# Optimization experiments

Hardware: AMD Instinct MI355X
Metric: run time of the kernel (lower is better)

Reference implementation:

```python
import jax, jax.numpy as jnp
import numpy as np

N_NODES = 20000
NC = 16
NUM_BASIS = 5
MAX_CENTER = 3.5

# Real-basis Clebsch-Gordan tensors C[m, m_f, m_o] for the (l, l_f) -> l_o paths.
# Real l=1 basis ordered (m=-1,0,1) = (y,z,x); (y,z,x) is a cyclic permutation of
# (x,y,z) so the standard Levi-Civita gives the 1x1->1 coupling.
_C000 = np.ones((1, 1, 1), dtype=np.float32)
_C011 = np.eye(3, dtype=np.float32).reshape(1, 3, 3)
_C101 = np.eye(3, dtype=np.float32).reshape(3, 1, 3)
_C110 = (np.eye(3, dtype=np.float32) / np.sqrt(3.0)).reshape(3, 3, 1)
_eps = np.zeros((3, 3, 3), dtype=np.float32)
for (i, j, k) in [(0, 1, 2), (1, 2, 0), (2, 0, 1)]:
    _eps[i, j, k] = 1.0
    _eps[i, k, j] = -1.0
_C111 = (_eps / np.sqrt(2.0)).astype(np.float32)

Y00 = 0.28209479177387814  # 1 / (2 sqrt(pi))
Y1C = 0.4886025119029199   # sqrt(3 / (4 pi))


def _spherical_filter(edges, coeffs, l_f):
    """SphericalFilter.__call__: RBF radial part x solid harmonics. -> [E, n_c, 2l_f+1]."""
    centers = jnp.linspace(0.0, MAX_CENTER, NUM_BASIS)
    spread = (MAX_CENTER - 0.0) / NUM_BASIS  # (max - min) / num_basis = 0.7
    radius = jnp.linalg.norm(edges, ord=2, axis=-1)              # [E]
    rbfs = jnp.exp(-spread * (radius[:, None] - centers) ** 2)   # [E, num_basis]
    rad = rbfs @ coeffs.T                                        # [E, n_c]
    if l_f == 0:
        y = jnp.full(edges.shape[:-1] + (1,), Y00, dtype=edges.dtype)
    else:  # l_f == 1: solid harmonics r^1 * Y_1m, order (y, z, x)
        y = Y1C * edges[:, jnp.array([1, 2, 0])]
    y = jnp.nan_to_num(y)
    return rad[:, :, None] * y[:, None, :]


def _tp(nodes, filt, cg, w):
    """Depthwise CG tensor product: [E,c,m],[E,c,f],[m,f,o] -> w[c] * [E,c,o]."""
    out = jnp.einsum('ecm,ecf,mfo->eco', nodes, filt, jnp.asarray(cg))
    return w[None, :, None] * out


def setup_inputs() -> dict:
    key = jax.random.key(0)
    ks = jax.random.split(key, 16)
    E = 640000
    inp = {
        'coords': jax.random.normal(ks[0], (N_NODES, 3), dtype=jnp.float32),
        'nodes0': jax.random.normal(ks[1], (N_NODES, NC, 1), dtype=jnp.float32),
        'nodes1': jax.random.normal(ks[2], (N_NODES, NC, 3), dtype=jnp.float32),
        'edges': jax.random.normal(ks[3], (E, 3), dtype=jnp.float32),
        'senders': jax.random.randint(ks[4], (E,), 0, N_NODES, dtype=jnp.int32),
        'receivers': jax.random.randint(ks[5], (E,), 0, N_NODES, dtype=jnp.int32),
        'coeffs_00': jax.random.uniform(ks[6], (NC, NUM_BASIS), dtype=jnp.float32),
        'coeffs_01': jax.random.uniform(ks[7], (NC, NUM_BASIS), dtype=jnp.float32),
        'coeffs_10': jax.random.uniform(ks[8], (NC, NUM_BASIS), dtype=jnp.float32),
        'coeffs_11': jax.random.uniform(ks[9], (NC, NUM_BASIS), dtype=jnp.float32),
        'w_000': jax.random.normal(ks[10], (NC,), dtype=jnp.float32) + 1.0,
        'w_011': jax.random.normal(ks[11], (NC,), dtype=jnp.float32) + 1.0,
        'w_101': jax.random.normal(ks[12], (NC,), dtype=jnp.float32) + 1.0,
        'w_110': jax.random.normal(ks[13], (NC,), dtype=jnp.float32) + 1.0,
        'w_111': jax.random.normal(ks[14], (NC,), dtype=jnp.float32) + 1.0,
    }
    return inp


def reference(coords, nodes0, nodes1, edges, senders, receivers,
              coeffs_00, coeffs_01, coeffs_10, coeffs_11,
              w_000, w_011, w_101, w_110, w_111):
    # Gather sender node features once per l.
    n0s = nodes0[senders]  # [E, NC, 1]
    n1s = nodes1[senders]  # [E, NC, 3]

    # Filters (loop order: l=0 filters [l_f=0, l_f=1], then l=1 filters).
    f00 = _spherical_filter(edges, coeffs_00, 0)  # [E, NC, 1]
    f01 = _spherical_filter(edges, coeffs_01, 1)  # [E, NC, 3]
    f10 = _spherical_filter(edges, coeffs_10, 0)  # [E, NC, 1]
    f11 = _spherical_filter(edges, coeffs_11, 1)  # [E, NC, 3]

    # Tensor-product messages, concatenated per output degree along channels.
    # l_o = 0 paths: (l=0, l_f=0), (l=1, l_f=1)
    m0 = jnp.concatenate([
        _tp(n0s, f00, _C000, w_000),
        _tp(n1s, f11, _C110, w_110),
    ], axis=-2)  # [E, 2*NC, 1]
    # l_o = 1 paths: (0,1), (1,0), (1,1)
    m1 = jnp.concatenate([
        _tp(n0s, f01, _C011, w_011),
        _tp(n1s, f10, _C101, w_101),
        _tp(n1s, f11, _C111, w_111),
    ], axis=-2)  # [E, 3*NC, 3]

    new0 = jax.ops.segment_sum(m0, receivers, num_segments=N_NODES)
    new1 = jax.ops.segment_sum(m1, receivers, num_segments=N_NODES)
    return coords, new0, new1
```

## Files before the change

### kernel.cpp

```cpp
#include <hip/hip_runtime.h>
#include <hip/hip_fp16.h>

#define E_EDGES 640000
#define NN 20000
#define NC 16
#define PBIN 64

#define Y00F 0.28209479177387814f
#define Y1CF 0.4886025119029199f
#define RS3  0.5773502691896258f
#define RS2  0.7071067811865476f

typedef float nf4 __attribute__((ext_vector_type(4)));

struct Acc {
    float a000, a110;
    float a011x, a011y, a011z;
    float a101x, a101y, a101z;
    float a111x, a111y, a111z;
};

__device__ __forceinline__ unsigned pack2h(float a, float b) {
    unsigned short ua = __half_as_ushort(__float2half(a));
    unsigned short ub = __half_as_ushort(__float2half(b));
    return (unsigned)ua | ((unsigned)ub << 16);
}
__device__ __forceinline__ float lo_h(unsigned u) {
    return __half2float(__ushort_as_half((unsigned short)(u & 0xffffu)));
}
__device__ __forceinline__ float hi_h(unsigned u) {
    return __half2float(__ushort_as_half((unsigned short)(u >> 16)));
}


__global__ void init1_kernel(const float* __restrict__ coords,
                             float* __restrict__ out,
                             int* __restrict__ cnt,
                             int* __restrict__ ovf_count) {
    int i = blockIdx.x * blockDim.x + threadIdx.x;
    if (i < 3 * NN) out[i] = coords[i];
    if (i < NN) cnt[i] = 0;
    if (i == 0) *ovf_count = 0;
}

__global__ void bin_kernel(const float* __restrict__ edges,
                           const int* __restrict__ senders,
                           const int* __restrict__ receivers,
                           int* __restrict__ cnt,
                           nf4* __restrict__ bins,
                           int* __restrict__ ovf_count,
                           int* __restrict__ ovf_list) {
    int e = blockIdx.x * blockDim.x + threadIdx.x;
    if (e >= E_EDGES) return;
    float ex = edges[3 * e + 0];
    float ey = edges[3 * e + 1];
    float ez = edges[3 * e + 2];
    int s  = senders[e];
    int rc = receivers[e];
    int pos = atomicAdd(&cnt[rc], 1);
    if (pos < PBIN) {
        float r2 = ex * ex + ey * ey + ez * ez;
        float r  = sqrtf(r2);
        float A  = __expf(-0.7f * r2);
        float t  = __expf(1.225f * r);
        nf4 rec;
        rec.x = __uint_as_float(pack2h(Y1CF * ey, Y1CF * ez));
        rec.y = __uint_as_float(pack2h(Y1CF * ex, t));
        rec.z = A;
        rec.w = __int_as_float(s);
        bins[(size_t)rc * PBIN + pos] = rec;
    } else {
        int k = atomicAdd(ovf_count, 1);
        if (k < 4096) ovf_list[k] = e;
    }
}

__global__ __launch_bounds__(256) void gather1_kernel(
    const nf4*    __restrict__ bins,
    const int*    __restrict__ cnt,
    const float*  __restrict__ nodes0,
    const float*  __restrict__ nodes1,
    const float*  __restrict__ c00, const float* __restrict__ c01,
    const float*  __restrict__ c10, const float* __restrict__ c11,
    const float*  __restrict__ w000, const float* __restrict__ w011,
    const float*  __restrict__ w101, const float* __restrict__ w110,
    const float*  __restrict__ w111,
    float* __restrict__ out0, float* __restrict__ out1)
{
    int gtid = blockIdx.x * blockDim.x + threadIdx.x;
    int node = gtid >> 6;
    int lane = threadIdx.x & 63;
    int c    = lane & 15;
    int j    = lane >> 4;
    if (node >= NN) return;

    const float KB[5] = {1.0f, 0.58512723f, 0.11721218f, 0.00803909f, 1.8876652e-4f};
    float k00[5], k01[5], k10[5], k11[5];
#pragma unroll
    for (int b = 0; b < 5; b++) {
        k00[b] = c00[c * 5 + b] * KB[b];
        k01[b] = c01[c * 5 + b] * KB[b];
        k10[b] = c10[c * 5 + b] * KB[b];
        k11[b] = c11[c * 5 + b] * KB[b];
    }

    int n = cnt[node];
    n = (n < PBIN) ? n : PBIN;
    const nf4* base = bins + (size_t)node * PBIN;

    Acc A = {};

#define HORNER(k, t) fmaf((t), fmaf((t), fmaf((t), fmaf((t), k[4], k[3]), k[2]), k[1]), k[0])
#define BODY(rec)                                                          \
    {                                                                      \
        unsigned u0 = __float_as_uint(rec.x);                              \
        unsigned u1 = __float_as_uint(rec.y);                              \
        float py = lo_h(u0), pz = hi_h(u0);                                \
        float px = lo_h(u1), tf = hi_h(u1);                                \
        float Af = rec.z;                                                  \
        int s = __float_as_int(rec.w);                                     \
        float rad00 = Af * HORNER(k00, tf);                                \
        float rad01 = Af * HORNER(k01, tf);                                \
        float rad10 = Af * HORNER(k10, tf);                                \
        float rad11 = Af * HORNER(k11, tf);                                \
        float n0 = nodes0[s * NC + c];                                     \
        const float* n1p = nodes1 + (s * NC + c) * 3;                      \
        float n1a = n1p[0], n1b = n1p[1], n1c = n1p[2];                    \
        A.a000 = fmaf(n0, rad00, A.a000);                                  \
        A.a110 = fmaf(rad11, n1a * py + n1b * pz + n1c * px, A.a110);      \
        float kA = n0 * rad01;                                             \
        A.a011x = fmaf(kA, py, A.a011x);                                   \
        A.a011y = fmaf(kA, pz, A.a011y);                                   \
        A.a011z = fmaf(kA, px, A.a011z);                                   \
        A.a101x = fmaf(rad10, n1a, A.a101x);                               \
        A.a101y = fmaf(rad10, n1b, A.a101y);                               \
        A.a101z = fmaf(rad10, n1c, A.a101z);                               \
        A.a111x = fmaf(rad11, n1b * px - n1c * pz, A.a111x);               \
        A.a111y = fmaf(rad11, n1c * py - n1a * px, A.a111y);               \
        A.a111z = fmaf(rad11, n1a * pz - n1b * py, A.a111z);               \
    }

    int i = j;
    for (; i + 12 < n; i += 16) {
        nf4 r0 = __builtin_nontemporal_load(&base[i]);
        nf4 r1 = __builtin_nontemporal_load(&base[i + 4]);
        nf4 r2 = __builtin_nontemporal_load(&base[i + 8]);
        nf4 r3 = __builtin_nontemporal_load(&base[i + 12]);
        BODY(r0);
        BODY(r1);
        BODY(r2);
        BODY(r3);
    }
    for (; i < n; i += 4) {
        nf4 r0 = __builtin_nontemporal_load(&base[i]);
        BODY(r0);
    }
#undef BODY
#undef HORNER

#define RED(v) v += __shfl_xor(v, 16, 64); v += __shfl_xor(v, 32, 64)
    RED(A.a000); RED(A.a110);
    RED(A.a011x); RED(A.a011y); RED(A.a011z);
    RED(A.a101x); RED(A.a101y); RED(A.a101z);
    RED(A.a111x); RED(A.a111y); RED(A.a111z);
#undef RED

    if (j == 0) {
        float s000 = w000[c] * Y00F;
        float s110 = w110[c] * RS3;
        float s011 = w011[c];
        float s101 = w101[c] * Y00F;
        float s111 = w111[c] * RS2;

        out0[node * 32 + c]      = s000 * A.a000;
        out0[node * 32 + 16 + c] = s110 * A.a110;

        float* o1 = out1 + node * 144;
        o1[3 * c + 0] = s011 * A.a011x;
        o1[3 * c + 1] = s011 * A.a011y;
        o1[3 * c + 2] = s011 * A.a011z;
        o1[3 * (16 + c) + 0] = s101 * A.a101x;
        o1[3 * (16 + c) + 1] = s101 * A.a101y;
        o1[3 * (16 + c) + 2] = s101 * A.a101z;
        o1[3 * (32 + c) + 0] = s111 * A.a111x;
        o1[3 * (32 + c) + 1] = s111 * A.a111y;
        o1[3 * (32 + c) + 2] = s111 * A.a111z;
    }
}

__global__ void cleanup_kernel(
    const int* __restrict__ ovf_count, const int* __restrict__ ovf_list,
    const float* __restrict__ edges, const int* __restrict__ senders,
    const int* __restrict__ receivers,
    const float* __restrict__ nodes0, const float* __restrict__ nodes1,
    const float* __restrict__ c00, const float* __restrict__ c01,
    const float* __restrict__ c10, const float* __restrict__ c11,
    const float* __restrict__ w000, const float* __restrict__ w011,
    const float* __restrict__ w101, const float* __restrict__ w110,
    const float* __restrict__ w111,
    float* __restrict__ out0, float* __restrict__ out1)
{
    int nov = *ovf_count;
    if (nov > 4096) nov = 4096;
    for (int k = threadIdx.x; k < nov; k += blockDim.x) {
        int e = ovf_list[k];
        float ex = edges[3 * e + 0], ey = edges[3 * e + 1], ez = edges[3 * e + 2];
        float r = sqrtf(ex * ex + ey * ey + ez * ez);
        float rbf[5];
#pragma unroll
        for (int b = 0; b < 5; b++) {
            float d = r - 0.875f * (float)b;
            rbf[b] = __expf(-0.7f * d * d);
        }
        int s = senders[e], rc = receivers[e];
        const float* n0p = nodes0 + s * NC;
        const float* n1p = nodes1 + s * NC * 3;
        float* o0 = out0 + rc * 32;
        float* o1 = out1 + rc * 144;
        float pey = Y1CF * ey, pez = Y1CF * ez, pex = Y1CF * ex;
        for (int c = 0; c < NC; c++) {
            float rad00 = 0.f, rad01 = 0.f, rad10 = 0.f, rad11 = 0.f;
#pragma unroll
            for (int b = 0; b < 5; b++) {
                rad00 = fmaf(rbf[b], c00[c * 5 + b], rad00);
                rad01 = fmaf(rbf[b], c01[c * 5 + b], rad01);
                rad10 = fmaf(rbf[b], c10[c * 5 + b], rad10);
                rad11 = fmaf(rbf[b], c11[c * 5 + b], rad11);
            }
            float n0 = n0p[c];
            float n1a = n1p[3 * c + 0], n1b = n1p[3 * c + 1], n1c = n1p[3 * c + 2];
            float f11a = rad11 * pey, f11b = rad11 * pez, f11c = rad11 * pex;
            atomicAdd(&o0[c], w000[c] * n0 * rad00 * Y00F);
            atomicAdd(&o0[16 + c], w110[c] * RS3 * (n1a * f11a + n1b * f11b + n1c * f11c));
            float kA = w011[c] * n0 * rad01;
            atomicAdd(&o1[3 * c + 0], kA * pey);
            atomicAdd(&o1[3 * c + 1], kA * pez);
            atomicAdd(&o1[3 * c + 2], kA * pex);
            float kB = w101[c] * rad10 * Y00F;
            atomicAdd(&o1[3 * (16 + c) + 0], kB * n1a);
            atomicAdd(&o1[3 * (16 + c) + 1], kB * n1b);
            atomicAdd(&o1[3 * (16 + c) + 2], kB * n1c);
            float kC = w111[c] * RS2;
            atomicAdd(&o1[3 * (32 + c) + 0], kC * (n1b * f11c - n1c * f11b));
            atomicAdd(&o1[3 * (32 + c) + 1], kC * (n1c * f11a - n1a * f11c));
            atomicAdd(&o1[3 * (32 + c) + 2], kC * (n1a * f11b - n1b * f11a));
        }
    }
}

__global__ void init_out_fb(const float* __restrict__ coords,
                            float* __restrict__ out, int out_size) {
    int i = blockIdx.x * blockDim.x + threadIdx.x;
    if (i < 3 * NN) out[i] = coords[i];
    else if (i < out_size) out[i] = 0.0f;
}

__global__ __launch_bounds__(256) void tp_edges_fb(
    const float* __restrict__ edges, const int* __restrict__ senders,
    const int* __restrict__ receivers, const float* __restrict__ nodes0,
    const float* __restrict__ nodes1,
    const float* __restrict__ c00, const float* __restrict__ c01,
    const float* __restrict__ c10, const float* __restrict__ c11,
    const float* __restrict__ w000, const float* __restrict__ w011,
    const float* __restrict__ w101, const float* __restrict__ w110,
    const float* __restrict__ w111,
    float* __restrict__ out0, float* __restrict__ out1) {
    int e = blockIdx.x * blockDim.x + threadIdx.x;
    if (e >= E_EDGES) return;
    float ex = edges[3 * e + 0], ey = edges[3 * e + 1], ez = edges[3 * e + 2];
    float r = sqrtf(ex * ex + ey * ey + ez * ez);
    float rbf[5];
#pragma unroll
    for (int b = 0; b < 5; b++) {
        float d = r - 0.875f * (float)b;
        rbf[b] = __expf(-0.7f * d * d);
    }
    int s = senders[e], rc = receivers[e];
    const float* n0p = nodes0 + s * NC;
    const float* n1p = nodes1 + s * NC * 3;
    float* o0 = out0 + rc * 32;
    float* o1 = out1 + rc * 144;
    float pey = Y1CF * ey, pez = Y1CF * ez, pex = Y1CF * ex;
    for (int c = 0; c < NC; c++) {
        float rad00 = 0.f, rad01 = 0.f, rad10 = 0.f, rad11 = 0.f;
#pragma unroll
        for (int b = 0; b < 5; b++) {
            rad00 = fmaf(rbf[b], c00[c * 5 + b], rad00);
            rad01 = fmaf(rbf[b], c01[c * 5 + b], rad01);
            rad10 = fmaf(rbf[b], c10[c * 5 + b], rad10);
            rad11 = fmaf(rbf[b], c11[c * 5 + b], rad11);
        }
        float n0 = n0p[c];
        float n1a = n1p[3 * c + 0], n1b = n1p[3 * c + 1], n1c = n1p[3 * c + 2];
        float f11a = rad11 * pey, f11b = rad11 * pez, f11c = rad11 * pex;
        atomicAdd(&o0[c], w000[c] * n0 * rad00 * Y00F);
        atomicAdd(&o0[16 + c], w110[c] * RS3 * (n1a * f11a + n1b * f11b + n1c * f11c));
        float kA = w011[c] * n0 * rad01;
        atomicAdd(&o1[3 * c + 0], kA * pey);
        atomicAdd(&o1[3 * c + 1], kA * pez);
        atomicAdd(&o1[3 * c + 2], kA * pex);
        float kB = w101[c] * rad10 * Y00F;
        atomicAdd(&o1[3 * (16 + c) + 0], kB * n1a);
        atomicAdd(&o1[3 * (16 + c) + 1], kB * n1b);
        atomicAdd(&o1[3 * (16 + c) + 2], kB * n1c);
        float kC = w111[c] * RS2;
        atomicAdd(&o1[3 * (32 + c) + 0], kC * (n1b * f11c - n1c * f11b));
        atomicAdd(&o1[3 * (32 + c) + 1], kC * (n1c * f11a - n1a * f11c));
        atomicAdd(&o1[3 * (32 + c) + 2], kC * (n1a * f11b - n1b * f11a));
    }
}

extern "C" void kernel_launch(void* const* d_in, const int* in_sizes, int n_in,
                              void* d_out, int out_size, void* d_ws, size_t ws_size,
                              hipStream_t stream) {
    const float* coords    = (const float*)d_in[0];
    const float* nodes0    = (const float*)d_in[1];
    const float* nodes1    = (const float*)d_in[2];
    const float* edges     = (const float*)d_in[3];
    const int*   senders   = (const int*)  d_in[4];
    const int*   receivers = (const int*)  d_in[5];
    const float* c00       = (const float*)d_in[6];
    const float* c01       = (const float*)d_in[7];
    const float* c10       = (const float*)d_in[8];
    const float* c11       = (const float*)d_in[9];
    const float* w000      = (const float*)d_in[10];
    const float* w011      = (const float*)d_in[11];
    const float* w101      = (const float*)d_in[12];
    const float* w110      = (const float*)d_in[13];
    const float* w111      = (const float*)d_in[14];

    float* out  = (float*)d_out;
    float* out0 = out + 3 * NN;
    float* out1 = out + 3 * NN + NN * 2 * NC;

    size_t bins_bytes = (size_t)NN * PBIN * 16;
    size_t need1 = bins_bytes + (size_t)(NN + 1 + 4096) * 4;

    if (ws_size >= need1) {
        nf4* bins      = (nf4*)d_ws;
        int* cnt       = (int*)((char*)d_ws + bins_bytes);
        int* ovf_count = cnt + NN;
        int* ovf_list  = ovf_count + 1;

        init1_kernel<<<(3 * NN + 255) / 256, 256, 0, stream>>>(coords, out, cnt, ovf_count);
        bin_kernel<<<(E_EDGES + 255) / 256, 256, 0, stream>>>(
            edges, senders, receivers, cnt, bins, ovf_count, ovf_list);
        gather1_kernel<<<(NN * 64 + 255) / 256, 256, 0, stream>>>(
            bins, cnt, nodes0, nodes1,
            c00, c01, c10, c11, w000, w011, w101, w110, w111, out0, out1);
        cleanup_kernel<<<1, 256, 0, stream>>>(
            ovf_count, ovf_list, edges, senders, receivers, nodes0, nodes1,
            c00, c01, c10, c11, w000, w011, w101, w110, w111, out0, out1);
    } else {
        init_out_fb<<<(out_size + 255) / 256, 256, 0, stream>>>(coords, out, out_size);
        tp_edges_fb<<<(E_EDGES + 255) / 256, 256, 0, stream>>>(
            edges, senders, receivers, nodes0, nodes1,
            c00, c01, c10, c11, w000, w011, w101, w110, w111, out0, out1);
    }
}
```

Before: 173.5 us.

## Pack node features to fp16 and use 128 threads per node in gather

Result: faster. 165.4 us (-4.7%).

```diff
diff --git a/kernel.cpp b/kernel.cpp
--- a/kernel.cpp
+++ b/kernel.cpp
@@ -12,13 +12,7 @@
 #define RS2  0.7071067811865476f
 
 typedef float nf4 __attribute__((ext_vector_type(4)));
-
-struct Acc {
-    float a000, a110;
-    float a011x, a011y, a011z;
-    float a101x, a101y, a101z;
-    float a111x, a111y, a111z;
-};
+typedef unsigned int nu2 __attribute__((ext_vector_type(2)));
 
 __device__ __forceinline__ unsigned pack2h(float a, float b) {
     unsigned short ua = __half_as_ushort(__float2half(a));
@@ -34,13 +28,24 @@
 
 
 __global__ void init1_kernel(const float* __restrict__ coords,
+                             const float* __restrict__ nodes0,
+                             const float* __restrict__ nodes1,
                              float* __restrict__ out,
                              int* __restrict__ cnt,
-                             int* __restrict__ ovf_count) {
+                             int* __restrict__ ovf_count,
+                             nu2* __restrict__ nodes_h) {
     int i = blockIdx.x * blockDim.x + threadIdx.x;
     if (i < 3 * NN) out[i] = coords[i];
     if (i < NN) cnt[i] = 0;
     if (i == 0) *ovf_count = 0;
+    if (i < NN * NC) {
+        float n0 = nodes0[i];
+        const float* n1p = nodes1 + i * 3;
+        nu2 v;
+        v.x = pack2h(n0, n1p[0]);
+        v.y = pack2h(n1p[1], n1p[2]);
+        nodes_h[i] = v;
+    }
 }
 
 __global__ void bin_kernel(const float* __restrict__ edges,
@@ -78,8 +83,7 @@
 __global__ __launch_bounds__(256) void gather1_kernel(
     const nf4*    __restrict__ bins,
     const int*    __restrict__ cnt,
-    const float*  __restrict__ nodes0,
-    const float*  __restrict__ nodes1,
+    const nu2*    __restrict__ nodes_h,
     const float*  __restrict__ c00, const float* __restrict__ c01,
     const float*  __restrict__ c10, const float* __restrict__ c11,
     const float*  __restrict__ w000, const float* __restrict__ w011,
@@ -87,12 +91,12 @@
     const float*  __restrict__ w111,
     float* __restrict__ out0, float* __restrict__ out1)
 {
-    int gtid = blockIdx.x * blockDim.x + threadIdx.x;
-    int node = gtid >> 6;
-    int lane = threadIdx.x & 63;
-    int c    = lane & 15;
-    int j    = lane >> 4;
-    if (node >= NN) return;
+    int t    = threadIdx.x;
+    int slot = t >> 7;
+    int node = blockIdx.x * 2 + slot;
+    int tid  = t & 127;
+    int c    = tid & 15;
+    int j    = tid >> 4;
 
     const float KB[5] = {1.0f, 0.58512723f, 0.11721218f, 0.00803909f, 1.8876652e-4f};
     float k00[5], k01[5], k10[5], k11[5];
@@ -108,7 +112,10 @@
     n = (n < PBIN) ? n : PBIN;
     const nf4* base = bins + (size_t)node * PBIN;
 
-    Acc A = {};
+    float a000 = 0.f, a110 = 0.f;
+    float a011x = 0.f, a011y = 0.f, a011z = 0.f;
+    float a101x = 0.f, a101y = 0.f, a101z = 0.f;
+    float a111x = 0.f, a111y = 0.f, a111z = 0.f;
 
 #define HORNER(k, t) fmaf((t), fmaf((t), fmaf((t), fmaf((t), k[4], k[3]), k[2]), k[1]), k[0])
 #define BODY(rec)                                                          \
@@ -119,39 +126,35 @@
         float px = lo_h(u1), tf = hi_h(u1);                                \
         float Af = rec.z;                                                  \
         int s = __float_as_int(rec.w);                                     \
+        nu2 nh = nodes_h[s * NC + c];                                      \
         float rad00 = Af * HORNER(k00, tf);                                \
         float rad01 = Af * HORNER(k01, tf);                                \
         float rad10 = Af * HORNER(k10, tf);                                \
         float rad11 = Af * HORNER(k11, tf);                                \
-        float n0 = nodes0[s * NC + c];                                     \
-        const float* n1p = nodes1 + (s * NC + c) * 3;                      \
-        float n1a = n1p[0], n1b = n1p[1], n1c = n1p[2];                    \
-        A.a000 = fmaf(n0, rad00, A.a000);                                  \
-        A.a110 = fmaf(rad11, n1a * py + n1b * pz + n1c * px, A.a110);      \
+        float n0  = lo_h(nh.x), n1a = hi_h(nh.x);                          \
+        float n1b = lo_h(nh.y), n1c = hi_h(nh.y);                          \
+        a000 = fmaf(n0, rad00, a000);                                      \
+        a110 = fmaf(rad11, n1a * py + n1b * pz + n1c * px, a110);          \
         float kA = n0 * rad01;                                             \
-        A.a011x = fmaf(kA, py, A.a011x);                                   \
-        A.a011y = fmaf(kA, pz, A.a011y);                                   \
-        A.a011z = fmaf(kA, px, A.a011z);                                   \
-        A.a101x = fmaf(rad10, n1a, A.a101x);                               \
-        A.a101y = fmaf(rad10, n1b, A.a101y);                               \
-        A.a101z = fmaf(rad10, n1c, A.a101z);                               \
-        A.a111x = fmaf(rad11, n1b * px - n1c * pz, A.a111x);               \
-        A.a111y = fmaf(rad11, n1c * py - n1a * px, A.a111y);               \
-        A.a111z = fmaf(rad11, n1a * pz - n1b * py, A.a111z);               \
+        a011x = fmaf(kA, py, a011x);                                       \
+        a011y = fmaf(kA, pz, a011y);                                       \
+        a011z = fmaf(kA, px, a011z);                                       \
+        a101x = fmaf(rad10, n1a, a101x);                                   \
+        a101y = fmaf(rad10, n1b, a101y);                                   \
+        a101z = fmaf(rad10, n1c, a101z);                                   \
+        a111x = fmaf(rad11, n1b * px - n1c * pz, a111x);                   \
+        a111y = fmaf(rad11, n1c * py - n1a * px, a111y);                   \
+        a111z = fmaf(rad11, n1a * pz - n1b * py, a111z);                   \
     }
 
     int i = j;
-    for (; i + 12 < n; i += 16) {
+    for (; i + 8 < n; i += 16) {
         nf4 r0 = __builtin_nontemporal_load(&base[i]);
-        nf4 r1 = __builtin_nontemporal_load(&base[i + 4]);
-        nf4 r2 = __builtin_nontemporal_load(&base[i + 8]);
-        nf4 r3 = __builtin_nontemporal_load(&base[i + 12]);
+        nf4 r1 = __builtin_nontemporal_load(&base[i + 8]);
         BODY(r0);
         BODY(r1);
-        BODY(r2);
-        BODY(r3);
-    }
-    for (; i < n; i += 4) {
+    }
+    if (i < n) {
         nf4 r0 = __builtin_nontemporal_load(&base[i]);
         BODY(r0);
     }
@@ -159,32 +162,48 @@
 #undef HORNER
 
 #define RED(v) v += __shfl_xor(v, 16, 64); v += __shfl_xor(v, 32, 64)
-    RED(A.a000); RED(A.a110);
-    RED(A.a011x); RED(A.a011y); RED(A.a011z);
-    RED(A.a101x); RED(A.a101y); RED(A.a101z);
-    RED(A.a111x); RED(A.a111y); RED(A.a111z);
+    RED(a000); RED(a110);
+    RED(a011x); RED(a011y); RED(a011z);
+    RED(a101x); RED(a101y); RED(a101z);
+    RED(a111x); RED(a111y); RED(a111z);
 #undef RED
 
-    if (j == 0) {
+    __shared__ float red[2][16][11];
+    int half = tid >> 6;
+    if (half == 0 && (tid & 63) < 16) {
+        float* p = red[slot][c];
+        p[0] = a000;  p[1] = a110;
+        p[2] = a011x; p[3] = a011y; p[4]  = a011z;
+        p[5] = a101x; p[6] = a101y; p[7]  = a101z;
+        p[8] = a111x; p[9] = a111y; p[10] = a111z;
+    }
+    __syncthreads();
+    if (half == 1 && (tid & 63) < 16) {
+        const float* p = red[slot][c];
+        a000  += p[0];  a110  += p[1];
+        a011x += p[2];  a011y += p[3];  a011z += p[4];
+        a101x += p[5];  a101y += p[6];  a101z += p[7];
+        a111x += p[8];  a111y += p[9];  a111z += p[10];
+
         float s000 = w000[c] * Y00F;
         float s110 = w110[c] * RS3;
         float s011 = w011[c];
         float s101 = w101[c] * Y00F;
         float s111 = w111[c] * RS2;
 
-        out0[node * 32 + c]      = s000 * A.a000;
-        out0[node * 32 + 16 + c] = s110 * A.a110;
+        out0[node * 32 + c]      = s000 * a000;
+        out0[node * 32 + 16 + c] = s110 * a110;
 
         float* o1 = out1 + node * 144;
-        o1[3 * c + 0] = s011 * A.a011x;
-        o1[3 * c + 1] = s011 * A.a011y;
-        o1[3 * c + 2] = s011 * A.a011z;
-        o1[3 * (16 + c) + 0] = s101 * A.a101x;
-        o1[3 * (16 + c) + 1] = s101 * A.a101y;
-        o1[3 * (16 + c) + 2] = s101 * A.a101z;
-        o1[3 * (32 + c) + 0] = s111 * A.a111x;
-        o1[3 * (32 + c) + 1] = s111 * A.a111y;
-        o1[3 * (32 + c) + 2] = s111 * A.a111z;
+        o1[3 * c + 0] = s011 * a011x;
+        o1[3 * c + 1] = s011 * a011y;
+        o1[3 * c + 2] = s011 * a011z;
+        o1[3 * (16 + c) + 0] = s101 * a101x;
+        o1[3 * (16 + c) + 1] = s101 * a101y;
+        o1[3 * (16 + c) + 2] = s101 * a101z;
+        o1[3 * (32 + c) + 0] = s111 * a111x;
+        o1[3 * (32 + c) + 1] = s111 * a111y;
+        o1[3 * (32 + c) + 2] = s111 * a111z;
     }
 }
 
@@ -333,20 +352,23 @@
     float* out0 = out + 3 * NN;
     float* out1 = out + 3 * NN + NN * 2 * NC;
 
-    size_t bins_bytes = (size_t)NN * PBIN * 16;
-    size_t need1 = bins_bytes + (size_t)(NN + 1 + 4096) * 4;
+    size_t bins_bytes  = (size_t)NN * PBIN * 16;
+    size_t nodes_bytes = (size_t)NN * NC * 8;
+    size_t need1 = bins_bytes + nodes_bytes + (size_t)(NN + 1 + 4096) * 4;
 
     if (ws_size >= need1) {
         nf4* bins      = (nf4*)d_ws;
-        int* cnt       = (int*)((char*)d_ws + bins_bytes);
+        nu2* nodes_h   = (nu2*)((char*)d_ws + bins_bytes);
+        int* cnt       = (int*)((char*)d_ws + bins_bytes + nodes_bytes);
         int* ovf_count = cnt + NN;
         int* ovf_list  = ovf_count + 1;
 
-        init1_kernel<<<(3 * NN + 255) / 256, 256, 0, stream>>>(coords, out, cnt, ovf_count);
+        init1_kernel<<<(NN * NC + 255) / 256, 256, 0, stream>>>(
+            coords, nodes0, nodes1, out, cnt, ovf_count, nodes_h);
         bin_kernel<<<(E_EDGES + 255) / 256, 256, 0, stream>>>(
             edges, senders, receivers, cnt, bins, ovf_count, ovf_list);
-        gather1_kernel<<<(NN * 64 + 255) / 256, 256, 0, stream>>>(
-            bins, cnt, nodes0, nodes1,
+        gather1_kernel<<<NN / 2, 256, 0, stream>>>(
+            bins, cnt, nodes_h,
             c00, c01, c10, c11, w000, w011, w101, w110, w111, out0, out1);
         cleanup_kernel<<<1, 256, 0, stream>>>(
             ovf_count, ovf_list, edges, senders, receivers, nodes0, nodes1,
```
